# Kernel tuning notes

Measured on AMD Instinct MI355X. Metric: run time of the kernel, lower is better.

Reference implementation:

```python
import jax, jax.numpy as jnp
import numpy as np

N = 100_000   # nodes
E = 3_200_000 # edges (avg degree 32)
D = 128       # feature dim
L = 3         # encoder layers (GIN convs)
K = 2         # MLP linear layers per GIN conv (channel_list [128,128,128])
G = 64        # graphs in batch
C = 4         # output classes
BN_EPS = 1e-5


def setup_inputs() -> dict:
    key = jax.random.key(0)
    ks = jax.random.split(key, 12)
    x = jax.random.normal(ks[0], (N, D), dtype=jnp.float32)
    edge_index = jax.random.randint(ks[1], (2, E), 0, N, dtype=jnp.int64)
    batch = jnp.sort(jax.random.randint(ks[2], (N,), 0, G, dtype=jnp.int64))
    # GIN MLP params: L convs x K linear layers each, all D->D
    Ws = jax.random.normal(ks[3], (L, K, D, D), dtype=jnp.float32) * 0.05
    bs = jax.random.normal(ks[4], (L, K, D), dtype=jnp.float32) * 0.02
    # BatchNorm (eval mode) params/buffers per MLP layer
    gammas = 1.0 + 0.1 * jax.random.normal(ks[5], (L, K, D), dtype=jnp.float32)
    betas = 0.1 * jax.random.normal(ks[6], (L, K, D), dtype=jnp.float32)
    run_means = 0.1 * jax.random.normal(ks[7], (L, K, D), dtype=jnp.float32)
    run_vars = jax.random.uniform(ks[8], (L, K, D), dtype=jnp.float32, minval=0.5, maxval=1.5)
    # final classifier
    lin_W = jax.random.normal(ks[9], (D, C), dtype=jnp.float32) * 0.05
    lin_b = jax.random.normal(ks[10], (C,), dtype=jnp.float32) * 0.02
    return {"x": x, "edge_index": edge_index, "batch": batch,
            "Ws": Ws, "bs": bs, "gammas": gammas, "betas": betas,
            "run_means": run_means, "run_vars": run_vars,
            "lin_W": lin_W, "lin_b": lin_b}


def reference(x, edge_index, batch, Ws, bs, gammas, betas, run_means, run_vars, lin_W, lin_b):
    src, dst = edge_index[0], edge_index[1]
    h = x
    for l in range(L):
        # GINConv (eps=0): h_i <- MLP(h_i + sum_{j->i} h_j)
        agg = jax.ops.segment_sum(h[src], dst, num_segments=N)  # [N, D]
        h = h + agg
        for k in range(K):
            # Linear -> BatchNorm(eval) -> ReLU (plain_last=False, dropout=0)
            y = h @ Ws[l, k] + bs[l, k]
            scale = gammas[l, k] / jnp.sqrt(run_vars[l, k] + BN_EPS)
            h = jax.nn.relu((y - run_means[l, k]) * scale + betas[l, k])
    pooled = jax.ops.segment_max(h, batch, num_segments=G)  # [G, D]
    logits = pooled @ lin_W + lin_b                          # [G, C]
    return jax.nn.log_softmax(logits, axis=-1)
```

## Files before the change

kernel.cpp:

```cpp
#include <hip/hip_runtime.h>
#include <stdint.h>

#define NN 100000
#define EE 3200000
#define DD 128
#define GG 64
#define CC 4
#define LLAYERS 3
#define KLIN 2
#define BN_EPS 1e-5f

#define BSH 8
#define NB ((NN + 255) >> BSH)
#define CHUNK3 8192
#define NBLK3 ((EE + CHUNK3 - 1) / CHUNK3)
#define STAGE_CAP 10240

#define HSP 136

typedef unsigned short u16;
typedef unsigned int u32;
typedef short bf16x8 __attribute__((ext_vector_type(8)));
typedef float f32x4 __attribute__((ext_vector_type(4)));

__device__ __forceinline__ float bflo(u32 u){ return __uint_as_float(u << 16); }
__device__ __forceinline__ float bfhi(u32 u){ return __uint_as_float(u & 0xffff0000u); }
__device__ __forceinline__ u16 f2bf(float f){
  u32 u = __float_as_uint(f);
  u32 r = u + 0x7fffu + ((u >> 16) & 1u);
  return (u16)(r >> 16);
}


__global__ __launch_bounds__(256) void bucket_hist(const int* __restrict__ dst,
                                                   int* __restrict__ bcount){
  __shared__ int lh[NB];
  for (int i = threadIdx.x; i < NB; i += 256) lh[i] = 0;
  __syncthreads();
  const int b0 = blockIdx.x * CHUNK3;
  const int cnt = min(CHUNK3, EE - b0);
  const int4* d4 = (const int4*)(dst + b0);
  const int n4 = cnt >> 2;
  for (int i = threadIdx.x; i < n4; i += 256) {
    int4 v = d4[i];
    atomicAdd(&lh[v.x >> BSH], 1);
    atomicAdd(&lh[v.y >> BSH], 1);
    atomicAdd(&lh[v.z >> BSH], 1);
    atomicAdd(&lh[v.w >> BSH], 1);
  }
  for (int i = (n4 << 2) + threadIdx.x; i < cnt; i += 256)
    atomicAdd(&lh[dst[b0 + i] >> BSH], 1);
  __syncthreads();
  for (int i = threadIdx.x; i < NB; i += 256)
    if (lh[i]) atomicAdd(&bcount[i], lh[i]);
}

__global__ __launch_bounds__(512) void bucket_scan(const int* __restrict__ bcount,
                                                   int* __restrict__ bofs,
                                                   int* __restrict__ gcur,
                                                   int* __restrict__ row_start){
  __shared__ int s[512];
  int t = threadIdx.x;
  int v = (t < NB) ? bcount[t] : 0;
  s[t] = v; __syncthreads();
  for (int off = 1; off < 512; off <<= 1) {
    int u = (t >= off) ? s[t - off] : 0;
    __syncthreads();
    s[t] += u;
    __syncthreads();
  }
  if (t < NB) { int e = s[t] - v; bofs[t] = e; gcur[t] = e; }
  if (t == 0) row_start[NN] = EE;
}

__global__ __launch_bounds__(256) void bucket_scatter(const int* __restrict__ src,
                                                      const int* __restrict__ dst,
                                                      int* __restrict__ gcur,
                                                      u32* __restrict__ rec){
  __shared__ int lh[NB];
  __shared__ int lbase[NB];
  const int b0 = blockIdx.x * CHUNK3;
  const int cnt = min(CHUNK3, EE - b0);
  const int n4 = cnt >> 2;
  const int4* s4 = (const int4*)(src + b0);
  const int4* d4 = (const int4*)(dst + b0);
  for (int i = threadIdx.x; i < NB; i += 256) lh[i] = 0;
  __syncthreads();
  for (int i = threadIdx.x; i < n4; i += 256) {
    int4 v = d4[i];
    atomicAdd(&lh[v.x >> BSH], 1);
    atomicAdd(&lh[v.y >> BSH], 1);
    atomicAdd(&lh[v.z >> BSH], 1);
    atomicAdd(&lh[v.w >> BSH], 1);
  }
  for (int i = (n4 << 2) + threadIdx.x; i < cnt; i += 256)
    atomicAdd(&lh[dst[b0 + i] >> BSH], 1);
  __syncthreads();
  for (int i = threadIdx.x; i < NB; i += 256) {
    int c = lh[i];
    lbase[i] = c ? atomicAdd(&gcur[i], c) : 0;
    lh[i] = 0;
  }
  __syncthreads();
  for (int i = threadIdx.x; i < n4; i += 256) {
    int4 ss = s4[i], dd = d4[i];
    {
      int bk = dd.x >> BSH;
      int pos = lbase[bk] + atomicAdd(&lh[bk], 1);
      rec[pos] = ((u32)ss.x << BSH) | (u32)(dd.x & 255);
    }
    {
      int bk = dd.y >> BSH;
      int pos = lbase[bk] + atomicAdd(&lh[bk], 1);
      rec[pos] = ((u32)ss.y << BSH) | (u32)(dd.y & 255);
    }
    {
      int bk = dd.z >> BSH;
      int pos = lbase[bk] + atomicAdd(&lh[bk], 1);
      rec[pos] = ((u32)ss.z << BSH) | (u32)(dd.z & 255);
    }
    {
      int bk = dd.w >> BSH;
      int pos = lbase[bk] + atomicAdd(&lh[bk], 1);
      rec[pos] = ((u32)ss.w << BSH) | (u32)(dd.w & 255);
    }
  }
  for (int i = (n4 << 2) + threadIdx.x; i < cnt; i += 256) {
    int d = dst[b0 + i];
    int bk = d >> BSH;
    int pos = lbase[bk] + atomicAdd(&lh[bk], 1);
    rec[pos] = ((u32)src[b0 + i] << BSH) | (u32)(d & 255);
  }
}

__global__ __launch_bounds__(256) void bucket_emit(const u32* __restrict__ rec,
                                                   const int* __restrict__ bofs,
                                                   const int* __restrict__ bcount,
                                                   int* __restrict__ row_start,
                                                   int* __restrict__ sorted_src){
  __shared__ int cnt[256];
  __shared__ int ofs[256];
  __shared__ int stage[STAGE_CAP];
  const int b = blockIdx.x, t = threadIdx.x;
  const int nodebase = b << BSH;
  const int nlocal = min(256, NN - nodebase);
  const int ebeg = bofs[b];
  const int ecnt = bcount[b];
  cnt[t] = 0;
  __syncthreads();
  for (int i = t; i < ecnt; i += 256)
    atomicAdd(&cnt[rec[ebeg + i] & 255u], 1);
  __syncthreads();
  int v = cnt[t];
  ofs[t] = v;
  __syncthreads();
  for (int off = 1; off < 256; off <<= 1) {
    int u = (t >= off) ? ofs[t - off] : 0;
    __syncthreads();
    ofs[t] += u;
    __syncthreads();
  }
  int excl = ofs[t] - v;
  if (t < nlocal) row_start[nodebase + t] = ebeg + excl;
  cnt[t] = excl;
  __syncthreads();
  for (int i = t; i < ecnt; i += 256) {
    u32 r = rec[ebeg + i];
    int pos = atomicAdd(&cnt[r & 255u], 1);
    if (pos < STAGE_CAP) stage[pos] = (int)(r >> BSH);
    else sorted_src[ebeg + pos] = (int)(r >> BSH);
  }
  __syncthreads();
  int lim = min(ecnt, STAGE_CAP);
  for (int i = t; i < lim; i += 256)
    sorted_src[ebeg + i] = stage[i];
}

__global__ __launch_bounds__(256) void prep_cast_kernel(const float* __restrict__ Ws,
    const float* __restrict__ bs, const float* __restrict__ gammas,
    const float* __restrict__ betas, const float* __restrict__ means,
    const float* __restrict__ vars,
    u16* __restrict__ Wt6, float* __restrict__ scale6, float* __restrict__ shift6,
    const float4* __restrict__ x, uint4* __restrict__ h){
  if (blockIdx.x < 6) {
    const int s = blockIdx.x;
    const float* W = Ws + (size_t)s * DD * DD;
    u16* Wt = Wt6 + (size_t)s * DD * DD;
    const int t = threadIdx.x;
    if (t < DD) {
      float sc = gammas[s*DD+t] * rsqrtf(vars[s*DD+t] + BN_EPS);
      scale6[s*DD+t] = sc;
      shift6[s*DD+t] = (bs[s*DD+t] - means[s*DD+t]) * sc + betas[s*DD+t];
    }
    for (int f = t; f < DD*DD; f += 256) {
      int j = f & 7, lane = (f >> 3) & 63, ks = (f >> 9) & 3, ct = f >> 11;
      int k = ks*32 + (lane >> 4)*8 + j;
      int n = ct*16 + (lane & 15);
      Wt[f] = f2bf(W[k*DD + n]);
    }
  } else {
    int i = (blockIdx.x - 6) * 256 + threadIdx.x;
    if (i < NN*DD/8) {
      float4 a = x[2*i], b = x[2*i+1];
      uint4 o;
      o.x = (u32)f2bf(a.x) | ((u32)f2bf(a.y) << 16);
      o.y = (u32)f2bf(a.z) | ((u32)f2bf(a.w) << 16);
      o.z = (u32)f2bf(b.x) | ((u32)f2bf(b.y) << 16);
      o.w = (u32)f2bf(b.z) | ((u32)f2bf(b.w) << 16);
      h[i] = o;
    }
  }
}

__global__ __launch_bounds__(256) void gin_layer(
    const u16* __restrict__ H, u16* __restrict__ O,
    const int* __restrict__ row_start, const int* __restrict__ sorted_src,
    const u16* __restrict__ W1t, const float* __restrict__ scale1, const float* __restrict__ shift1,
    const u16* __restrict__ W2t, const float* __restrict__ scale2, const float* __restrict__ shift2)
{
  __shared__ u16 HS[16][HSP];
  __shared__ u16 YS[16][HSP];

  const int tid = threadIdx.x;
  const int base = blockIdx.x * 16;
  const uint4* hp = (const uint4*)H;

  {
    const int g = tid >> 4, l16 = tid & 15;
    const int node = base + g;
    uint4 v = hp[(size_t)node*16 + l16];
    float a0=bflo(v.x), a1=bfhi(v.x), a2=bflo(v.y), a3=bfhi(v.y);
    float a4=bflo(v.z), a5=bfhi(v.z), a6=bflo(v.w), a7=bfhi(v.w);
    float b0=0.f,b1=0.f,b2=0.f,b3=0.f,b4=0.f,b5=0.f,b6=0.f,b7=0.f;
    float c0=0.f,c1=0.f,c2=0.f,c3=0.f,c4=0.f,c5=0.f,c6=0.f,c7=0.f;
    float d0=0.f,d1=0.f,d2=0.f,d3=0.f,d4=0.f,d5=0.f,d6=0.f,d7=0.f;
    int e = row_start[node];
    const int end = row_start[node + 1];
    for (; e + 3 < end; e += 4) {
      int s0 = sorted_src[e],   s1 = sorted_src[e+1];
      int s2 = sorted_src[e+2], s3 = sorted_src[e+3];
      uint4 u0 = hp[(size_t)s0*16 + l16];
      uint4 u1 = hp[(size_t)s1*16 + l16];
      uint4 u2 = hp[(size_t)s2*16 + l16];
      uint4 u3 = hp[(size_t)s3*16 + l16];
      a0 += bflo(u0.x); a1 += bfhi(u0.x); a2 += bflo(u0.y); a3 += bfhi(u0.y);
      a4 += bflo(u0.z); a5 += bfhi(u0.z); a6 += bflo(u0.w); a7 += bfhi(u0.w);
      b0 += bflo(u1.x); b1 += bfhi(u1.x); b2 += bflo(u1.y); b3 += bfhi(u1.y);
      b4 += bflo(u1.z); b5 += bfhi(u1.z); b6 += bflo(u1.w); b7 += bfhi(u1.w);
      c0 += bflo(u2.x); c1 += bfhi(u2.x); c2 += bflo(u2.y); c3 += bfhi(u2.y);
      c4 += bflo(u2.z); c5 += bfhi(u2.z); c6 += bflo(u2.w); c7 += bfhi(u2.w);
      d0 += bflo(u3.x); d1 += bfhi(u3.x); d2 += bflo(u3.y); d3 += bfhi(u3.y);
      d4 += bflo(u3.z); d5 += bfhi(u3.z); d6 += bflo(u3.w); d7 += bfhi(u3.w);
    }
    for (; e < end; ++e) {
      int s0 = sorted_src[e];
      uint4 u0 = hp[(size_t)s0*16 + l16];
      a0 += bflo(u0.x); a1 += bfhi(u0.x); a2 += bflo(u0.y); a3 += bfhi(u0.y);
      a4 += bflo(u0.z); a5 += bfhi(u0.z); a6 += bflo(u0.w); a7 += bfhi(u0.w);
    }
    a0 += b0+c0+d0; a1 += b1+c1+d1; a2 += b2+c2+d2; a3 += b3+c3+d3;
    a4 += b4+c4+d4; a5 += b5+c5+d5; a6 += b6+c6+d6; a7 += b7+c7+d7;
    uint4 w;
    w.x = (u32)f2bf(a0) | ((u32)f2bf(a1) << 16);
    w.y = (u32)f2bf(a2) | ((u32)f2bf(a3) << 16);
    w.z = (u32)f2bf(a4) | ((u32)f2bf(a5) << 16);
    w.w = (u32)f2bf(a6) | ((u32)f2bf(a7) << 16);
    *(uint4*)&HS[g][l16*8] = w;
  }
  __syncthreads();

  const int wave = tid >> 6, lane = tid & 63;
  const int ln15 = lane & 15, quad = lane >> 4;

  {
    bf16x8 af[4];
    #pragma unroll
    for (int ks = 0; ks < 4; ++ks)
      af[ks] = *(const bf16x8*)&HS[ln15][ks*32 + quad*8];
    f32x4 acc[2];
    acc[0] = (f32x4){0.f,0.f,0.f,0.f};
    acc[1] = (f32x4){0.f,0.f,0.f,0.f};
    #pragma unroll
    for (int ks = 0; ks < 4; ++ks) {
      #pragma unroll
      for (int j = 0; j < 2; ++j) {
        const int ct = wave*2 + j;
        bf16x8 bf = *(const bf16x8*)(W1t + (((ct*4 + ks)*64 + lane) << 3));
        acc[j] = __builtin_amdgcn_mfma_f32_16x16x32_bf16(af[ks], bf, acc[j], 0, 0, 0);
      }
    }
    #pragma unroll
    for (int j = 0; j < 2; ++j) {
      const int col = (wave*2 + j)*16 + ln15;
      const float sc = scale1[col], sh = shift1[col];
      #pragma unroll
      for (int reg = 0; reg < 4; ++reg)
        YS[quad*4 + reg][col] = f2bf(fmaxf(acc[j][reg]*sc + sh, 0.f));
    }
  }
  __syncthreads();

  {
    bf16x8 af[4];
    #pragma unroll
    for (int ks = 0; ks < 4; ++ks)
      af[ks] = *(const bf16x8*)&YS[ln15][ks*32 + quad*8];
    f32x4 acc[2];
    acc[0] = (f32x4){0.f,0.f,0.f,0.f};
    acc[1] = (f32x4){0.f,0.f,0.f,0.f};
    #pragma unroll
    for (int ks = 0; ks < 4; ++ks) {
      #pragma unroll
      for (int j = 0; j < 2; ++j) {
        const int ct = wave*2 + j;
        bf16x8 bf = *(const bf16x8*)(W2t + (((ct*4 + ks)*64 + lane) << 3));
        acc[j] = __builtin_amdgcn_mfma_f32_16x16x32_bf16(af[ks], bf, acc[j], 0, 0, 0);
      }
    }
    #pragma unroll
    for (int j = 0; j < 2; ++j) {
      const int col = (wave*2 + j)*16 + ln15;
      const float sc = scale2[col], sh = shift2[col];
      #pragma unroll
      for (int reg = 0; reg < 4; ++reg) {
        const int row = base + quad*4 + reg;
        O[(size_t)row * DD + col] = f2bf(fmaxf(acc[j][reg]*sc + sh, 0.f));
      }
    }
  }
}

__global__ __launch_bounds__(256) void pool_classify(const u16* __restrict__ h,
    const int* __restrict__ batch, const float* __restrict__ lw,
    const float* __restrict__ lb, float* __restrict__ out){
  __shared__ float red[256 * 8];
  __shared__ float P[DD];
  __shared__ int range[2];
  const int g = blockIdx.x, tid = threadIdx.x;
  if (tid < 2) {
    int target = g + tid;
    int lo = 0, hi = NN;
    while (lo < hi) { int mid = (lo + hi) >> 1; if (batch[mid] < target) lo = mid + 1; else hi = mid; }
    range[tid] = lo;
  }
  __syncthreads();
  const int beg = range[0], end = range[1];
  const int rg = tid >> 4, l16 = tid & 15;
  const uint4* hp = (const uint4*)h;
  float m0=0.f,m1=0.f,m2=0.f,m3=0.f,m4=0.f,m5=0.f,m6=0.f,m7=0.f;
  for (int n = beg + rg; n < end; n += 16) {
    uint4 u = hp[(size_t)n * 16 + l16];
    m0 = fmaxf(m0, bflo(u.x)); m1 = fmaxf(m1, bfhi(u.x));
    m2 = fmaxf(m2, bflo(u.y)); m3 = fmaxf(m3, bfhi(u.y));
    m4 = fmaxf(m4, bflo(u.z)); m5 = fmaxf(m5, bfhi(u.z));
    m6 = fmaxf(m6, bflo(u.w)); m7 = fmaxf(m7, bfhi(u.w));
  }
  float* r = &red[tid * 8];
  r[0]=m0; r[1]=m1; r[2]=m2; r[3]=m3; r[4]=m4; r[5]=m5; r[6]=m6; r[7]=m7;
  __syncthreads();
  #pragma unroll
  for (int off = 8; off > 0; off >>= 1) {
    if (rg < off) {
      float* o = &red[(tid + off*16) * 8];
      #pragma unroll
      for (int i = 0; i < 8; ++i) r[i] = fmaxf(r[i], o[i]);
    }
    __syncthreads();
  }
  if (rg == 0) {
    #pragma unroll
    for (int i = 0; i < 8; ++i) P[l16*8 + i] = r[i];
  }
  __syncthreads();
  if (tid < 64) {
    float x0 = P[tid];
    float x1 = P[tid + 64];
    float4 wA = *(const float4*)(lw + tid*4);
    float4 wB = *(const float4*)(lw + (tid+64)*4);
    float a0 = x0*wA.x + x1*wB.x;
    float a1 = x0*wA.y + x1*wB.y;
    float a2 = x0*wA.z + x1*wB.z;
    float a3 = x0*wA.w + x1*wB.w;
    #pragma unroll
    for (int off = 32; off > 0; off >>= 1) {
      a0 += __shfl_down(a0, off);
      a1 += __shfl_down(a1, off);
      a2 += __shfl_down(a2, off);
      a3 += __shfl_down(a3, off);
    }
    if (tid == 0) {
      float l0 = a0 + lb[0];
      float l1 = a1 + lb[1];
      float l2 = a2 + lb[2];
      float l3 = a3 + lb[3];
      float m = fmaxf(fmaxf(l0,l1), fmaxf(l2,l3));
      float s = expf(l0-m)+expf(l1-m)+expf(l2-m)+expf(l3-m);
      float lse = logf(s) + m;
      out[g*4+0] = l0 - lse;
      out[g*4+1] = l1 - lse;
      out[g*4+2] = l2 - lse;
      out[g*4+3] = l3 - lse;
    }
  }
}

extern "C" void kernel_launch(void* const* d_in, const int* in_sizes, int n_in,
                              void* d_out, int out_size, void* d_ws, size_t ws_size,
                              hipStream_t stream) {
  const float* x     = (const float*)d_in[0];
  const int* ei      = (const int*)d_in[1];
  const int* batch   = (const int*)d_in[2];
  const float* Ws    = (const float*)d_in[3];
  const float* bs    = (const float*)d_in[4];
  const float* gammas= (const float*)d_in[5];
  const float* betas = (const float*)d_in[6];
  const float* means = (const float*)d_in[7];
  const float* vars  = (const float*)d_in[8];
  const float* lw    = (const float*)d_in[9];
  const float* lb    = (const float*)d_in[10];
  float* out = (float*)d_out;

  u16* hA = (u16*)d_ws;
  u16* hB = hA + (size_t)NN * DD;
  float* scale6 = (float*)(hB + (size_t)NN * DD);
  float* shift6 = scale6 + 6 * DD;
  int* row_start  = (int*)(shift6 + 6 * DD);
  int* bcount     = row_start + NN + 2;
  int* bofs       = bcount + NB;
  int* gcur       = bofs + NB;
  int* sorted_src = gcur + NB + 3;
  u16* Wt6 = (u16*)(((uintptr_t)(sorted_src + EE) + 63) & ~(uintptr_t)63);
  u32* rec = (u32*)hA;

  const int* srcIdx = ei;
  const int* dstIdx = ei + EE;

  hipMemsetAsync(bcount, 0, NB * sizeof(int), stream);
  bucket_hist<<<NBLK3, 256, 0, stream>>>(dstIdx, bcount);
  bucket_scan<<<1, 512, 0, stream>>>(bcount, bofs, gcur, row_start);
  bucket_scatter<<<NBLK3, 256, 0, stream>>>(srcIdx, dstIdx, gcur, rec);
  bucket_emit<<<NB, 256, 0, stream>>>(rec, bofs, bcount, row_start, sorted_src);

  prep_cast_kernel<<<6 + (NN*DD/8 + 255)/256, 256, 0, stream>>>(
      Ws, bs, gammas, betas, means, vars, Wt6, scale6, shift6,
      (const float4*)x, (uint4*)hA);

  u16* cur = hA;
  u16* tmp = hB;
  const int layer_grid = NN / 16;
  for (int l = 0; l < LLAYERS; ++l) {
    int s0 = l*KLIN + 0, s1 = l*KLIN + 1;
    gin_layer<<<layer_grid, 256, 0, stream>>>(cur, tmp, row_start, sorted_src,
        Wt6 + (size_t)s0*DD*DD, scale6 + s0*DD, shift6 + s0*DD,
        Wt6 + (size_t)s1*DD*DD, scale6 + s1*DD, shift6 + s1*DD);
    u16* t = cur; cur = tmp; tmp = t;
  }

  pool_classify<<<GG, 256, 0, stream>>>(cur, batch, lw, lb, out);
}
```

Before: 612.4 us.

## Fuse input cast into histogram and weight prep into scan; widen pooling

Merges the fp32-to-bf16 cast of x into the edge histogram kernel and the weight transpose plus BN folding into the bucket scan kernel, removing one launch. The weight transpose now stages W in LDS so global reads are coalesced. The edge chunk size is halved, giving histogram and scatter more blocks, and pooling runs with 512 threads. Because h is now written before the scatter, the radix record buffer moves out of hA into separate workspace, which needs about 12.8 MB more scratch space.

```diff
diff --git a/kernel.cpp b/kernel.cpp
--- a/kernel.cpp
+++ b/kernel.cpp
@@ -12,8 +12,8 @@
 
 #define BSH 8
 #define NB ((NN + 255) >> BSH)
-#define CHUNK3 8192
-#define NBLK3 ((EE + CHUNK3 - 1) / CHUNK3)
+#define CH 4096
+#define NH ((EE + CH - 1) / CH)
 #define STAGE_CAP 10240
 
 #define HSP 136
@@ -31,46 +31,88 @@
   return (u16)(r >> 16);
 }
 
-
-__global__ __launch_bounds__(256) void bucket_hist(const int* __restrict__ dst,
-                                                   int* __restrict__ bcount){
+__global__ __launch_bounds__(256) void hist_cast(const int* __restrict__ dst,
+                                                 int* __restrict__ bcount,
+                                                 const float4* __restrict__ x,
+                                                 uint4* __restrict__ h){
   __shared__ int lh[NB];
-  for (int i = threadIdx.x; i < NB; i += 256) lh[i] = 0;
-  __syncthreads();
-  const int b0 = blockIdx.x * CHUNK3;
-  const int cnt = min(CHUNK3, EE - b0);
-  const int4* d4 = (const int4*)(dst + b0);
-  const int n4 = cnt >> 2;
-  for (int i = threadIdx.x; i < n4; i += 256) {
-    int4 v = d4[i];
-    atomicAdd(&lh[v.x >> BSH], 1);
-    atomicAdd(&lh[v.y >> BSH], 1);
-    atomicAdd(&lh[v.z >> BSH], 1);
-    atomicAdd(&lh[v.w >> BSH], 1);
-  }
-  for (int i = (n4 << 2) + threadIdx.x; i < cnt; i += 256)
-    atomicAdd(&lh[dst[b0 + i] >> BSH], 1);
-  __syncthreads();
-  for (int i = threadIdx.x; i < NB; i += 256)
-    if (lh[i]) atomicAdd(&bcount[i], lh[i]);
-}
-
-__global__ __launch_bounds__(512) void bucket_scan(const int* __restrict__ bcount,
-                                                   int* __restrict__ bofs,
-                                                   int* __restrict__ gcur,
-                                                   int* __restrict__ row_start){
+  if (blockIdx.x < NH) {
+    for (int i = threadIdx.x; i < NB; i += 256) lh[i] = 0;
+    __syncthreads();
+    const int b0 = blockIdx.x * CH;
+    const int cnt = min(CH, EE - b0);
+    const int4* d4 = (const int4*)(dst + b0);
+    const int n4 = cnt >> 2;
+    for (int i = threadIdx.x; i < n4; i += 256) {
+      int4 v = d4[i];
+      atomicAdd(&lh[v.x >> BSH], 1);
+      atomicAdd(&lh[v.y >> BSH], 1);
+      atomicAdd(&lh[v.z >> BSH], 1);
+      atomicAdd(&lh[v.w >> BSH], 1);
+    }
+    for (int i = (n4 << 2) + threadIdx.x; i < cnt; i += 256)
+      atomicAdd(&lh[dst[b0 + i] >> BSH], 1);
+    __syncthreads();
+    for (int i = threadIdx.x; i < NB; i += 256)
+      if (lh[i]) atomicAdd(&bcount[i], lh[i]);
+  } else {
+    int i = (blockIdx.x - NH) * 256 + threadIdx.x;
+    if (i < NN*DD/8) {
+      float4 a = x[2*i], b = x[2*i+1];
+      uint4 o;
+      o.x = (u32)f2bf(a.x) | ((u32)f2bf(a.y) << 16);
+      o.y = (u32)f2bf(a.z) | ((u32)f2bf(a.w) << 16);
+      o.z = (u32)f2bf(b.x) | ((u32)f2bf(b.y) << 16);
+      o.w = (u32)f2bf(b.z) | ((u32)f2bf(b.w) << 16);
+      h[i] = o;
+    }
+  }
+}
+
+__global__ __launch_bounds__(512) void scan_prep(const int* __restrict__ bcount,
+    int* __restrict__ bofs, int* __restrict__ gcur, int* __restrict__ row_start,
+    const float* __restrict__ Ws, const float* __restrict__ bs,
+    const float* __restrict__ gammas, const float* __restrict__ betas,
+    const float* __restrict__ means, const float* __restrict__ vars,
+    u16* __restrict__ Wt6, float* __restrict__ scale6, float* __restrict__ shift6){
+  __shared__ float WS[64 * DD];
   __shared__ int s[512];
-  int t = threadIdx.x;
-  int v = (t < NB) ? bcount[t] : 0;
-  s[t] = v; __syncthreads();
-  for (int off = 1; off < 512; off <<= 1) {
-    int u = (t >= off) ? s[t - off] : 0;
-    __syncthreads();
-    s[t] += u;
-    __syncthreads();
-  }
-  if (t < NB) { int e = s[t] - v; bofs[t] = e; gcur[t] = e; }
-  if (t == 0) row_start[NN] = EE;
+  const int t = threadIdx.x;
+  if (blockIdx.x == 0) {
+    int v = (t < NB) ? bcount[t] : 0;
+    s[t] = v; __syncthreads();
+    for (int off = 1; off < 512; off <<= 1) {
+      int u = (t >= off) ? s[t - off] : 0;
+      __syncthreads();
+      s[t] += u;
+      __syncthreads();
+    }
+    if (t < NB) { int e = s[t] - v; bofs[t] = e; gcur[t] = e; }
+    if (t == 0) row_start[NN] = EE;
+  } else {
+    const int sl = blockIdx.x - 1;
+    const float* W = Ws + (size_t)sl * DD * DD;
+    u16* Wt = Wt6 + (size_t)sl * DD * DD;
+    if (t < DD) {
+      float sc = gammas[sl*DD+t] * rsqrtf(vars[sl*DD+t] + BN_EPS);
+      scale6[sl*DD+t] = sc;
+      shift6[sl*DD+t] = (bs[sl*DD+t] - means[sl*DD+t]) * sc + betas[sl*DD+t];
+    }
+    #pragma unroll
+    for (int p = 0; p < 2; ++p) {
+      __syncthreads();
+      const float4* srcp = (const float4*)(W + p * 64 * DD);
+      float4* dstp = (float4*)WS;
+      for (int i = t; i < 64 * DD / 4; i += 512) dstp[i] = srcp[i];
+      __syncthreads();
+      for (int f = t; f < DD*DD; f += 512) {
+        int j = f & 7, lane = (f >> 3) & 63, ks = (f >> 9) & 3, ct = f >> 11;
+        int k = ks*32 + (lane >> 4)*8 + j;
+        if ((k >> 6) == p)
+          Wt[f] = f2bf(WS[(k & 63)*DD + ct*16 + (lane & 15)]);
+      }
+    }
+  }
 }
 
 __global__ __launch_bounds__(256) void bucket_scatter(const int* __restrict__ src,
@@ -79,8 +121,8 @@
                                                       u32* __restrict__ rec){
   __shared__ int lh[NB];
   __shared__ int lbase[NB];
-  const int b0 = blockIdx.x * CHUNK3;
-  const int cnt = min(CHUNK3, EE - b0);
+  const int b0 = blockIdx.x * CH;
+  const int cnt = min(CH, EE - b0);
   const int n4 = cnt >> 2;
   const int4* s4 = (const int4*)(src + b0);
   const int4* d4 = (const int4*)(dst + b0);
@@ -174,42 +216,6 @@
   int lim = min(ecnt, STAGE_CAP);
   for (int i = t; i < lim; i += 256)
     sorted_src[ebeg + i] = stage[i];
-}
-
-__global__ __launch_bounds__(256) void prep_cast_kernel(const float* __restrict__ Ws,
-    const float* __restrict__ bs, const float* __restrict__ gammas,
-    const float* __restrict__ betas, const float* __restrict__ means,
-    const float* __restrict__ vars,
-    u16* __restrict__ Wt6, float* __restrict__ scale6, float* __restrict__ shift6,
-    const float4* __restrict__ x, uint4* __restrict__ h){
-  if (blockIdx.x < 6) {
-    const int s = blockIdx.x;
-    const float* W = Ws + (size_t)s * DD * DD;
-    u16* Wt = Wt6 + (size_t)s * DD * DD;
-    const int t = threadIdx.x;
-    if (t < DD) {
-      float sc = gammas[s*DD+t] * rsqrtf(vars[s*DD+t] + BN_EPS);
-      scale6[s*DD+t] = sc;
-      shift6[s*DD+t] = (bs[s*DD+t] - means[s*DD+t]) * sc + betas[s*DD+t];
-    }
-    for (int f = t; f < DD*DD; f += 256) {
-      int j = f & 7, lane = (f >> 3) & 63, ks = (f >> 9) & 3, ct = f >> 11;
-      int k = ks*32 + (lane >> 4)*8 + j;
-      int n = ct*16 + (lane & 15);
-      Wt[f] = f2bf(W[k*DD + n]);
-    }
-  } else {
-    int i = (blockIdx.x - 6) * 256 + threadIdx.x;
-    if (i < NN*DD/8) {
-      float4 a = x[2*i], b = x[2*i+1];
-      uint4 o;
-      o.x = (u32)f2bf(a.x) | ((u32)f2bf(a.y) << 16);
-      o.y = (u32)f2bf(a.z) | ((u32)f2bf(a.w) << 16);
-      o.z = (u32)f2bf(b.x) | ((u32)f2bf(b.y) << 16);
-      o.w = (u32)f2bf(b.z) | ((u32)f2bf(b.w) << 16);
-      h[i] = o;
-    }
-  }
 }
 
 __global__ __launch_bounds__(256) void gin_layer(
@@ -330,10 +336,10 @@
   }
 }
 
-__global__ __launch_bounds__(256) void pool_classify(const u16* __restrict__ h,
+__global__ __launch_bounds__(512) void pool_classify(const u16* __restrict__ h,
     const int* __restrict__ batch, const float* __restrict__ lw,
     const float* __restrict__ lb, float* __restrict__ out){
-  __shared__ float red[256 * 8];
+  __shared__ float red[512 * 8];
   __shared__ float P[DD];
   __shared__ int range[2];
   const int g = blockIdx.x, tid = threadIdx.x;
@@ -348,7 +354,7 @@
   const int rg = tid >> 4, l16 = tid & 15;
   const uint4* hp = (const uint4*)h;
   float m0=0.f,m1=0.f,m2=0.f,m3=0.f,m4=0.f,m5=0.f,m6=0.f,m7=0.f;
-  for (int n = beg + rg; n < end; n += 16) {
+  for (int n = beg + rg; n < end; n += 32) {
     uint4 u = hp[(size_t)n * 16 + l16];
     m0 = fmaxf(m0, bflo(u.x)); m1 = fmaxf(m1, bfhi(u.x));
     m2 = fmaxf(m2, bflo(u.y)); m3 = fmaxf(m3, bfhi(u.y));
@@ -359,7 +365,7 @@
   r[0]=m0; r[1]=m1; r[2]=m2; r[3]=m3; r[4]=m4; r[5]=m5; r[6]=m6; r[7]=m7;
   __syncthreads();
   #pragma unroll
-  for (int off = 8; off > 0; off >>= 1) {
+  for (int off = 16; off > 0; off >>= 1) {
     if (rg < off) {
       float* o = &red[(tid + off*16) * 8];
       #pragma unroll
@@ -429,21 +435,19 @@
   int* bofs       = bcount + NB;
   int* gcur       = bofs + NB;
   int* sorted_src = gcur + NB + 3;
-  u16* Wt6 = (u16*)(((uintptr_t)(sorted_src + EE) + 63) & ~(uintptr_t)63);
-  u32* rec = (u32*)hA;
+  u32* rec        = (u32*)(sorted_src + EE);
+  u16* Wt6 = (u16*)(((uintptr_t)(rec + EE) + 63) & ~(uintptr_t)63);
 
   const int* srcIdx = ei;
   const int* dstIdx = ei + EE;
 
   hipMemsetAsync(bcount, 0, NB * sizeof(int), stream);
-  bucket_hist<<<NBLK3, 256, 0, stream>>>(dstIdx, bcount);
-  bucket_scan<<<1, 512, 0, stream>>>(bcount, bofs, gcur, row_start);
-  bucket_scatter<<<NBLK3, 256, 0, stream>>>(srcIdx, dstIdx, gcur, rec);
+  hist_cast<<<NH + (NN*DD/8 + 255)/256, 256, 0, stream>>>(
+      dstIdx, bcount, (const float4*)x, (uint4*)hA);
+  scan_prep<<<7, 512, 0, stream>>>(bcount, bofs, gcur, row_start,
+      Ws, bs, gammas, betas, means, vars, Wt6, scale6, shift6);
+  bucket_scatter<<<NH, 256, 0, stream>>>(srcIdx, dstIdx, gcur, rec);
   bucket_emit<<<NB, 256, 0, stream>>>(rec, bofs, bcount, row_start, sorted_src);
-
-  prep_cast_kernel<<<6 + (NN*DD/8 + 255)/256, 256, 0, stream>>>(
-      Ws, bs, gammas, betas, means, vars, Wt6, scale6, shift6,
-      (const float4*)x, (uint4*)hA);
 
   u16* cur = hA;
   u16* tmp = hB;
@@ -456,5 +460,5 @@
     u16* t = cur; cur = tmp; tmp = t;
   }
 
-  pool_classify<<<GG, 256, 0, stream>>>(cur, batch, lw, lb, out);
-}
+  pool_classify<<<GG, 512, 0, stream>>>(cur, batch, lw, lb, out);
+}
```

Result: no change. 617.3 us (+0.8%).
